# Optimization experiments

Hardware: AMD Instinct MI355X
Metric: run time of the kernel (lower is better)

## Reference

```python
import jax, jax.numpy as jnp
import numpy as np

N_NODES = 100000
N_EDGES = 3200000
IN_DIM = 128
EMB_DIM = 128


def _glorot(key, shape):
    fan_in, fan_out = shape
    lim = jnp.sqrt(6.0 / (fan_in + fan_out))
    return jax.random.uniform(key, shape, jnp.float32, -lim, lim)


def setup_inputs() -> dict:
    key = jax.random.key(0)
    k1, k2, k3, k4, k5 = jax.random.split(key, 5)
    label_vectors = jax.random.normal(k1, (N_NODES, IN_DIM), jnp.float32)
    edge_index = jax.random.randint(k2, (2, N_EDGES), 0, N_NODES, jnp.int64)
    edge_weight = jax.random.uniform(k3, (N_EDGES,), jnp.float32)
    W1 = _glorot(k4, (IN_DIM, EMB_DIM))
    b1 = jnp.zeros((EMB_DIM,), jnp.float32)
    W2 = _glorot(k5, (EMB_DIM, EMB_DIM))
    b2 = jnp.zeros((EMB_DIM,), jnp.float32)
    return {"label_vectors": label_vectors, "edge_index": edge_index,
            "edge_weight": edge_weight, "W1": W1, "b1": b1, "W2": W2, "b2": b2}


def _gcn_layer(x, W, b, row, col, norm, n):
    # PyG GCNConv: h = x @ W; out[col] += norm * h[row]; out += b
    h = x @ W                                   # [N, d_out]
    msg = h[row] * norm[:, None]                # [E+N, d_out] gather + scale
    out = jax.ops.segment_sum(msg, col, num_segments=n)  # scatter-add
    return out + b


def reference(label_vectors, edge_index, edge_weight, W1, b1, W2, b2):
    n = label_vectors.shape[0]
    loops = jnp.arange(n, dtype=edge_index.dtype)
    row = jnp.concatenate([edge_index[0], loops])
    col = jnp.concatenate([edge_index[1], loops])
    ew = jnp.concatenate([edge_weight, jnp.ones((n,), edge_weight.dtype)])
    # symmetric normalization: deg computed over target index (col)
    deg = jax.ops.segment_sum(ew, col, num_segments=n)
    dinv = jnp.where(deg > 0, jax.lax.rsqrt(jnp.maximum(deg, 1e-38)), 0.0)
    norm = dinv[row] * ew * dinv[col]
    x = _gcn_layer(label_vectors, W1, b1, row, col, norm, n)
    x = jax.nn.relu(x)
    x = _gcn_layer(x, W2, b2, row, col, norm, n)
    return x
```

## Files before the change

kernel.cpp:

```cpp
#include <hip/hip_runtime.h>
#include <hip/hip_bf16.h>

typedef __hip_bfloat16 bf16;
#define DIM 128

static __device__ __forceinline__ float b2f_lo(unsigned u) {
  return __uint_as_float(u << 16);
}
static __device__ __forceinline__ float b2f_hi(unsigned u) {
  return __uint_as_float(u & 0xffff0000u);
}
static __device__ __forceinline__ unsigned short f2b(float f) {
  union { float f; unsigned u; } uf; uf.f = f;
  unsigned lsb = (uf.u >> 16) & 1u;
  unsigned r = uf.u + 0x7fffu + lsb;
  return (unsigned short)(r >> 16);
}

__global__ void k_probe(const int* __restrict__ ei, int* __restrict__ flag) {
  __shared__ int s;
  if (threadIdx.x == 0) s = 0;
  __syncthreads();
  int v = 0;
#pragma unroll
  for (int j = 0; j < 8; ++j) v |= ei[2 * (threadIdx.x * 8 + j) + 1];
  if (v) atomicOr(&s, 1);
  __syncthreads();
  if (threadIdx.x == 0) *flag = (s == 0) ? 1 : 0;
}

__global__ void k_init(unsigned long long* __restrict__ packed, int n) {
  int i = blockIdx.x * blockDim.x + threadIdx.x;
  if (i < n) packed[i] = 0ULL;
}

__global__ __launch_bounds__(256) void k_gemm_deg(
    const float* __restrict__ X, const float* __restrict__ W,
    bf16* __restrict__ H,
    const int* __restrict__ ei, const int* __restrict__ flag,
    const float* __restrict__ ew,
    unsigned long long* __restrict__ packed,
    unsigned short* __restrict__ rank,
    int n, int nE) {
  __shared__ float Xs[32][36];
  __shared__ float Ws[32][DIM];
  const int t = threadIdx.x;
  const int row0 = blockIdx.x * 32;
  const int jc = (t & 31) * 4;
  const int ir = (t >> 5) * 4;

  const bool w64 = (*flag != 0);
  unsigned long long olds[8];
#pragma unroll
  for (int j = 0; j < 8; ++j) {
    int e = (j * (int)gridDim.x + (int)blockIdx.x) * 256 + t;
    if (e < nE) {
      int c = w64 ? (int)((const long long*)ei)[(size_t)nE + e] : ei[(size_t)nE + e];
      unsigned fx = __float2uint_rn(ew[e] * 16777216.0f);
      olds[j] = atomicAdd(&packed[c], (1ULL << 32) | (unsigned long long)fx);
    }
  }

  float acc[4][4] = {};
  for (int kb = 0; kb < DIM; kb += 32) {
    for (int i = t; i < 32 * 32; i += 256) {
      int k = i >> 5;
      int j = (i & 31) * 4;
      *(float4*)&Ws[k][j] = *(const float4*)(W + (size_t)(kb + k) * DIM + j);
    }
    {
      int i = t;
      int r = i >> 3;
      int kk = (i & 7) * 4;
      float4 v = make_float4(0.f, 0.f, 0.f, 0.f);
      if (row0 + r < n) v = *(const float4*)(X + (size_t)(row0 + r) * DIM + kb + kk);
      Xs[kk + 0][r] = v.x; Xs[kk + 1][r] = v.y;
      Xs[kk + 2][r] = v.z; Xs[kk + 3][r] = v.w;
    }
    __syncthreads();
#pragma unroll 8
    for (int k = 0; k < 32; ++k) {
      float4 xv = *(const float4*)&Xs[k][ir];
      float4 wv = *(const float4*)&Ws[k][jc];
      const float* xp = (const float*)&xv;
      const float* wp = (const float*)&wv;
#pragma unroll
      for (int a = 0; a < 4; ++a)
#pragma unroll
        for (int b = 0; b < 4; ++b)
          acc[a][b] = fmaf(xp[a], wp[b], acc[a][b]);
    }
    __syncthreads();
  }
#pragma unroll
  for (int a = 0; a < 4; ++a) {
    int r = row0 + ir + a;
    if (r < n) {
      unsigned o0 = (unsigned)f2b(acc[a][0]) | ((unsigned)f2b(acc[a][1]) << 16);
      unsigned o1 = (unsigned)f2b(acc[a][2]) | ((unsigned)f2b(acc[a][3]) << 16);
      *(uint2*)(H + (size_t)r * DIM + jc) = make_uint2(o0, o1);
    }
  }

#pragma unroll
  for (int j = 0; j < 8; ++j) {
    int e = (j * (int)gridDim.x + (int)blockIdx.x) * 256 + t;
    if (e < nE) rank[e] = (unsigned short)(olds[j] >> 32);
  }
}

__global__ void k_bsum(const unsigned long long* __restrict__ packed,
                       float* __restrict__ dinv, int* __restrict__ bsum, int n) {
  __shared__ int sd[256];
  int i = blockIdx.x * 256 + threadIdx.x;
  int c = 0;
  if (i < n) {
    unsigned long long v = packed[i];
    c = (int)(v >> 32);
    dinv[i] = rsqrtf(1.0f + (float)(unsigned)(v & 0xffffffffu) *
                                (1.0f / 16777216.0f));
  }
  sd[threadIdx.x] = c;
  __syncthreads();
  for (int off = 128; off > 0; off >>= 1) {
    if (threadIdx.x < off) sd[threadIdx.x] += sd[threadIdx.x + off];
    __syncthreads();
  }
  if (threadIdx.x == 0) bsum[blockIdx.x] = sd[0];
}

__global__ void k_bscan(int* __restrict__ bsum, int nb) {
  __shared__ int sd[1024];
  int t = threadIdx.x;
  int v = (t < nb) ? bsum[t] : 0;
  sd[t] = v;
  __syncthreads();
  for (int off = 1; off < 1024; off <<= 1) {
    int val = (t >= off) ? sd[t - off] : 0;
    __syncthreads();
    sd[t] += val;
    __syncthreads();
  }
  if (t < nb) bsum[t] = sd[t] - v;
}

__global__ void k_emit(const unsigned long long* __restrict__ packed,
                       const int* __restrict__ bstart,
                       int* __restrict__ rowptr, int n) {
  __shared__ int sd[256];
  int i = blockIdx.x * 256 + threadIdx.x;
  int c = (i < n) ? (int)(packed[i] >> 32) : 0;
  sd[threadIdx.x] = c;
  __syncthreads();
  for (int off = 1; off < 256; off <<= 1) {
    int val = (threadIdx.x >= off) ? sd[threadIdx.x - off] : 0;
    __syncthreads();
    sd[threadIdx.x] += val;
    __syncthreads();
  }
  if (i < n) rowptr[i + 1] = bstart[blockIdx.x] + sd[threadIdx.x];
  if (blockIdx.x == 0 && threadIdx.x == 0) rowptr[0] = 0;
}

__global__ void k_scatter(const int* __restrict__ ei, const int* __restrict__ flag,
                          const float* __restrict__ ew, const float* __restrict__ dinv,
                          const int* __restrict__ rowptr,
                          const unsigned short* __restrict__ rank,
                          uint2* __restrict__ pairA, int nE) {
  int e = blockIdx.x * blockDim.x + threadIdx.x;
  if (e < nE) {
    int r, c;
    if (*flag) {
      r = (int)((const long long*)ei)[e];
      c = (int)((const long long*)ei)[(size_t)nE + e];
    } else {
      r = ei[e];
      c = ei[(size_t)nE + e];
    }
    float nm = dinv[r] * ew[e];
    int p = rowptr[c] + (int)rank[e];
    pairA[p] = make_uint2((unsigned)r, __float_as_uint(nm));
  }
}

__global__ __launch_bounds__(256) void k_agg_gemm(const bf16* __restrict__ H,
    const int* __restrict__ rowptr, const uint2* __restrict__ pairA,
    const float* __restrict__ dinv, const float* __restrict__ bias,
    const float* __restrict__ W2, bf16* __restrict__ H2, int n) {
  __shared__ float x2s[DIM][36];
  __shared__ float Ws[32][DIM];
  const int t = threadIdx.x;
  const int wid = t >> 6;
  const int lane = t & 63;
  const int base = blockIdx.x * 32;
  const unsigned* Hw = (const unsigned*)H;
  const float2 bv = ((const float2*)bias)[lane];

  for (int i = 0; i < 8; ++i) {
    const int r = wid * 8 + i;
    const int node = __builtin_amdgcn_readfirstlane(base + r);
    if (node < n) {
      float di = dinv[node];
      unsigned hv = Hw[(size_t)node * 64 + lane];
      float a0 = di * b2f_lo(hv);
      float a1 = di * b2f_hi(hv);
      float b0 = 0.f, b1v = 0.f, c0 = 0.f, c1 = 0.f, d0 = 0.f, d1 = 0.f;
      const int s = rowptr[node], e = rowptr[node + 1];
      for (int p = s; p < e; p += 16) {
        uint2 pr[16];
#pragma unroll
        for (int j = 0; j < 16; ++j) {
          int q = p + j;
          q = (q < e) ? q : (e - 1);
          pr[j] = pairA[q];
        }
        unsigned g[16];
#pragma unroll
        for (int j = 0; j < 16; ++j) g[j] = Hw[(size_t)pr[j].x * 64 + lane];
#pragma unroll
        for (int j = 0; j < 16; ++j) {
          float w = (p + j < e) ? __uint_as_float(pr[j].y) : 0.f;
          float lo = b2f_lo(g[j]), hi = b2f_hi(g[j]);
          switch (j & 3) {
            case 0: a0 = fmaf(w, lo, a0); a1 = fmaf(w, hi, a1); break;
            case 1: b0 = fmaf(w, lo, b0); b1v = fmaf(w, hi, b1v); break;
            case 2: c0 = fmaf(w, lo, c0); c1 = fmaf(w, hi, c1); break;
            default: d0 = fmaf(w, lo, d0); d1 = fmaf(w, hi, d1); break;
          }
        }
      }
      a0 += b0 + c0 + d0;
      a1 += b1v + c1 + d1;
      a0 = fmaxf(fmaf(di, a0, bv.x), 0.f);
      a1 = fmaxf(fmaf(di, a1, bv.y), 0.f);
      x2s[2 * lane][r]     = a0;
      x2s[2 * lane + 1][r] = a1;
    }
  }
  __syncthreads();

  const int jc = (t & 31) * 4;
  const int ir = (t >> 5) * 4;
  float acc[4][4] = {};
  for (int kb = 0; kb < DIM; kb += 32) {
    for (int i = t; i < 32 * 32; i += 256) {
      int k = i >> 5;
      int j = (i & 31) * 4;
      *(float4*)&Ws[k][j] = *(const float4*)(W2 + (size_t)(kb + k) * DIM + j);
    }
    __syncthreads();
#pragma unroll 8
    for (int k = 0; k < 32; ++k) {
      float4 xv = *(const float4*)&x2s[kb + k][ir];
      float4 wv = *(const float4*)&Ws[k][jc];
      const float* xp = (const float*)&xv;
      const float* wp = (const float*)&wv;
#pragma unroll
      for (int a = 0; a < 4; ++a)
#pragma unroll
        for (int b = 0; b < 4; ++b)
          acc[a][b] = fmaf(xp[a], wp[b], acc[a][b]);
    }
    __syncthreads();
  }
#pragma unroll
  for (int a = 0; a < 4; ++a) {
    int r = base + ir + a;
    if (r < n) {
      unsigned o0 = (unsigned)f2b(acc[a][0]) | ((unsigned)f2b(acc[a][1]) << 16);
      unsigned o1 = (unsigned)f2b(acc[a][2]) | ((unsigned)f2b(acc[a][3]) << 16);
      *(uint2*)(H2 + (size_t)r * DIM + jc) = make_uint2(o0, o1);
    }
  }
}

__global__ __launch_bounds__(256) void k_agg(const bf16* __restrict__ H,
    const int* __restrict__ rowptr, const uint2* __restrict__ pairA,
    const float* __restrict__ dinv, const float* __restrict__ bias,
    float* __restrict__ out, int n) {
  int node = __builtin_amdgcn_readfirstlane(blockIdx.x * 4 + (threadIdx.x >> 6));
  if (node >= n) return;
  int lane = threadIdx.x & 63;
  const unsigned* Hw = (const unsigned*)H;
  float di = dinv[node];
  unsigned hv = Hw[(size_t)node * 64 + lane];
  float a0 = di * b2f_lo(hv);
  float a1 = di * b2f_hi(hv);
  float b0 = 0.f, b1v = 0.f, c0 = 0.f, c1 = 0.f, d0 = 0.f, d1 = 0.f;
  const int s = rowptr[node], e = rowptr[node + 1];
  for (int p = s; p < e; p += 16) {
    uint2 pr[16];
#pragma unroll
    for (int j = 0; j < 16; ++j) {
      int q = p + j;
      q = (q < e) ? q : (e - 1);
      pr[j] = pairA[q];
    }
    unsigned g[16];
#pragma unroll
    for (int j = 0; j < 16; ++j) g[j] = Hw[(size_t)pr[j].x * 64 + lane];
#pragma unroll
    for (int j = 0; j < 16; ++j) {
      float w = (p + j < e) ? __uint_as_float(pr[j].y) : 0.f;
      float lo = b2f_lo(g[j]), hi = b2f_hi(g[j]);
      switch (j & 3) {
        case 0: a0 = fmaf(w, lo, a0); a1 = fmaf(w, hi, a1); break;
        case 1: b0 = fmaf(w, lo, b0); b1v = fmaf(w, hi, b1v); break;
        case 2: c0 = fmaf(w, lo, c0); c1 = fmaf(w, hi, c1); break;
        default: d0 = fmaf(w, lo, d0); d1 = fmaf(w, hi, d1); break;
      }
    }
  }
  a0 += b0 + c0 + d0;
  a1 += b1v + c1 + d1;
  float2 bv = ((const float2*)bias)[lane];
  a0 = fmaf(di, a0, bv.x);
  a1 = fmaf(di, a1, bv.y);
  ((float2*)out)[(size_t)node * 64 + lane] = make_float2(a0, a1);
}

extern "C" void kernel_launch(void* const* d_in, const int* in_sizes, int n_in,
                              void* d_out, int out_size, void* d_ws, size_t ws_size,
                              hipStream_t stream) {
  const float* X  = (const float*)d_in[0];
  const int*   ei = (const int*)d_in[1];
  const float* ew = (const float*)d_in[2];
  const float* W1 = (const float*)d_in[3];
  const float* b1 = (const float*)d_in[4];
  const float* W2 = (const float*)d_in[5];
  const float* b2 = (const float*)d_in[6];
  const int N = in_sizes[0] / DIM;
  const int E = in_sizes[2];

  char* ws = (char*)d_ws;
  size_t off = 0;
  auto alloc = [&](size_t bytes) -> void* {
    void* p = ws + off;
    off = (off + bytes + 255) & ~(size_t)255;
    return p;
  };
  int*   flag  = (int*)  alloc(4);
  unsigned long long* packed = (unsigned long long*)alloc((size_t)N * 8);
  float* dinv  = (float*)alloc((size_t)N * 4);
  int*   rowptr= (int*)  alloc((size_t)(N + 1) * 4);
  int*   bsum  = (int*)  alloc((size_t)1024 * 4);
  unsigned short* rnk = (unsigned short*)alloc((size_t)E * 2);
  uint2* pairA = (uint2*)alloc((size_t)E * 8);
  bf16*  h     = (bf16*) alloc((size_t)N * DIM * 2);
  bf16*  h2    = (bf16*) alloc((size_t)N * DIM * 2);
  (void)ws_size; (void)n_in; (void)out_size;

  int bN  = (N + 255) / 256;
  int bE  = (E + 255) / 256;
  int gGemm = (N + 31) / 32;
  int gAgg  = (N + 3) / 4;

  k_probe   <<<1, 256, 0, stream>>>(ei, flag);
  k_init    <<<bN, 256, 0, stream>>>(packed, N);
  k_gemm_deg<<<gGemm, 256, 0, stream>>>(X, W1, h, ei, flag, ew, packed, rnk, N, E);
  k_bsum    <<<bN, 256, 0, stream>>>(packed, dinv, bsum, N);
  k_bscan   <<<1, 1024, 0, stream>>>(bsum, bN);
  k_emit    <<<bN, 256, 0, stream>>>(packed, bsum, rowptr, N);
  k_scatter <<<bE, 256, 0, stream>>>(ei, flag, ew, dinv, rowptr, rnk, pairA, E);

  k_agg_gemm<<<gGemm, 256, 0, stream>>>(h, rowptr, pairA, dinv, b1, W2, h2, N);
  k_agg     <<<gAgg, 256, 0, stream>>>(h2, rowptr, pairA, dinv, b2, (float*)d_out, N);
}
```

Before: 666.3 us.

## Split degree atomics and GEMM into interleaved specialized blocks

The fused GEMM+degree kernel now assigns every third block to a dedicated 'flood' role. Those blocks do the per-edge atomic degree and count accumulation and write each edge's rank immediately. The other blocks do only the X@W1 tile. Previously every block did 8 atomics per thread, held the results in registers through its GEMM tile, and stored the ranks at the end. The goal is to let the atomic-bound and compute-bound work run concurrently in separate blocks, and to cut register pressure in the GEMM blocks. The cost is a larger grid, with some blocks that exit early.

Result: faster. 643.1 us (-3.5%).

```diff
diff --git a/kernel.cpp b/kernel.cpp
--- a/kernel.cpp
+++ b/kernel.cpp
@@ -34,33 +34,44 @@
   if (i < n) packed[i] = 0ULL;
 }
 
-__global__ __launch_bounds__(256) void k_gemm_deg(
+__global__ __launch_bounds__(256) void k_mega(
     const float* __restrict__ X, const float* __restrict__ W,
     bf16* __restrict__ H,
     const int* __restrict__ ei, const int* __restrict__ flag,
     const float* __restrict__ ew,
     unsigned long long* __restrict__ packed,
     unsigned short* __restrict__ rank,
-    int n, int nE) {
+    int n, int nE, int gFlood) {
   __shared__ float Xs[32][36];
   __shared__ float Ws[32][DIM];
   const int t = threadIdx.x;
-  const int row0 = blockIdx.x * 32;
+  const int bid = blockIdx.x;
+
+  if (bid % 3 == 1) {
+    const int fid = bid / 3;
+    if (fid < gFlood) {
+      const bool w64 = (*flag != 0);
+#pragma unroll
+      for (int j = 0; j < 8; ++j) {
+        int e = (j * gFlood + fid) * 256 + t;
+        if (e < nE) {
+          int c = w64 ? (int)((const long long*)ei)[(size_t)nE + e]
+                      : ei[(size_t)nE + e];
+          unsigned fx = __float2uint_rn(ew[e] * 16777216.0f);
+          unsigned long long old =
+              atomicAdd(&packed[c], (1ULL << 32) | (unsigned long long)fx);
+          rank[e] = (unsigned short)(old >> 32);
+        }
+      }
+    }
+    return;
+  }
+
+  const int gid = (bid % 3 == 0) ? (bid / 3) * 2 : (bid / 3) * 2 + 1;
+  const int row0 = gid * 32;
+  if (row0 >= n) return;
   const int jc = (t & 31) * 4;
   const int ir = (t >> 5) * 4;
-
-  const bool w64 = (*flag != 0);
-  unsigned long long olds[8];
-#pragma unroll
-  for (int j = 0; j < 8; ++j) {
-    int e = (j * (int)gridDim.x + (int)blockIdx.x) * 256 + t;
-    if (e < nE) {
-      int c = w64 ? (int)((const long long*)ei)[(size_t)nE + e] : ei[(size_t)nE + e];
-      unsigned fx = __float2uint_rn(ew[e] * 16777216.0f);
-      olds[j] = atomicAdd(&packed[c], (1ULL << 32) | (unsigned long long)fx);
-    }
-  }
-
   float acc[4][4] = {};
   for (int kb = 0; kb < DIM; kb += 32) {
     for (int i = t; i < 32 * 32; i += 256) {
@@ -69,9 +80,8 @@
       *(float4*)&Ws[k][j] = *(const float4*)(W + (size_t)(kb + k) * DIM + j);
     }
     {
-      int i = t;
-      int r = i >> 3;
-      int kk = (i & 7) * 4;
+      int r = t >> 3;
+      int kk = (t & 7) * 4;
       float4 v = make_float4(0.f, 0.f, 0.f, 0.f);
       if (row0 + r < n) v = *(const float4*)(X + (size_t)(row0 + r) * DIM + kb + kk);
       Xs[kk + 0][r] = v.x; Xs[kk + 1][r] = v.y;
@@ -100,12 +110,6 @@
       unsigned o1 = (unsigned)f2b(acc[a][2]) | ((unsigned)f2b(acc[a][3]) << 16);
       *(uint2*)(H + (size_t)r * DIM + jc) = make_uint2(o0, o1);
     }
-  }
-
-#pragma unroll
-  for (int j = 0; j < 8; ++j) {
-    int e = (j * (int)gridDim.x + (int)blockIdx.x) * 256 + t;
-    if (e < nE) rank[e] = (unsigned short)(olds[j] >> 32);
   }
 }
 
@@ -353,11 +357,14 @@
   int bN  = (N + 255) / 256;
   int bE  = (E + 255) / 256;
   int gGemm = (N + 31) / 32;
+  int gFlood = (E + 2047) / 2048;
+  int gMega = gGemm + gFlood;
   int gAgg  = (N + 3) / 4;
 
   k_probe   <<<1, 256, 0, stream>>>(ei, flag);
   k_init    <<<bN, 256, 0, stream>>>(packed, N);
-  k_gemm_deg<<<gGemm, 256, 0, stream>>>(X, W1, h, ei, flag, ew, packed, rnk, N, E);
+  k_mega    <<<gMega, 256, 0, stream>>>(X, W1, h, ei, flag, ew, packed, rnk,
+                                        N, E, gFlood);
   k_bsum    <<<bN, 256, 0, stream>>>(packed, dinv, bsum, N);
   k_bscan   <<<1, 1024, 0, stream>>>(bsum, bN);
   k_emit    <<<bN, 256, 0, stream>>>(packed, bsum, rowptr, N);
```
